# Performance work log

Measured on AMD Instinct MI355X. Metric: run time of the kernel, lower is better.

The kernel has to match this reference:

```python
import jax, jax.numpy as jnp
import numpy as np
from jax import lax

B, C_IN, N, C_OUT, K = 8, 64, 4096, 64, 20
EPS = 1e-5
NEG_SLOPE = 0.2


def setup_inputs() -> dict:
    key = jax.random.key(0)
    k1, k2, k3, k4, k5, k6 = jax.random.split(key, 6)
    x = jax.random.normal(k1, (B, C_IN, N), dtype=jnp.float32)
    # Conv2d(2*C_in, C_out, kernel_size=1, bias=False) -> weight (C_out, 2*C_in)
    W = jax.random.normal(k2, (C_OUT, 2 * C_IN), dtype=jnp.float32) * (1.0 / np.sqrt(2 * C_IN))
    gamma = jax.random.normal(k3, (C_OUT,), dtype=jnp.float32) * 0.1 + 1.0
    beta = jax.random.normal(k4, (C_OUT,), dtype=jnp.float32) * 0.1
    running_mean = jax.random.normal(k5, (C_OUT,), dtype=jnp.float32) * 0.1
    running_var = jax.random.uniform(k6, (C_OUT,), dtype=jnp.float32, minval=0.5, maxval=1.5)
    return {"x": x, "W": W, "gamma": gamma, "beta": beta,
            "running_mean": running_mean, "running_var": running_var}


def reference(x, W, gamma, beta, running_mean, running_var):
    # x: (B, C, N)
    # ---- KNN graph: pairwise squared distances, top-k nearest (includes self) ----
    xx = jnp.sum(x * x, axis=1)                       # (B, N)
    inner = jnp.einsum('bcn,bcm->bnm', x, x)          # (B, N, N)
    d2 = xx[:, :, None] - 2.0 * inner + xx[:, None, :]  # (B, N, N)
    _, idx = lax.top_k(-d2, K)                        # (B, N, K) int32 indices

    # ---- gather neighbor features ----
    xt = jnp.transpose(x, (0, 2, 1))                  # (B, N, C)
    neighbors = jax.vmap(lambda feats, i: feats[i])(xt, idx)  # (B, N, K, C)
    central = xt[:, :, None, :]                       # (B, N, 1, C) broadcast over K

    # ---- edge features: [x_i, x_j - x_i] -> (B, N, K, 2C) ----
    edge = jnp.concatenate(
        [jnp.broadcast_to(central, (B, N, K, C_IN)), neighbors - central], axis=-1)

    # ---- 1x1 conv (pointwise matmul) + BatchNorm (eval mode) + LeakyReLU ----
    h = jnp.einsum('bnkc,oc->bnko', edge, W)          # (B, N, K, C_out)
    inv_std = lax.rsqrt(running_var + EPS)
    h = (h - running_mean) * (inv_std * gamma) + beta
    h = jnp.where(h >= 0, h, NEG_SLOPE * h)           # LeakyReLU(0.2)

    # ---- max over k neighbors, return (B, C_out, N) ----
    out = jnp.max(h, axis=2)                          # (B, N, C_out)
    return jnp.transpose(out, (0, 2, 1))
```

## Files before the change

### kernel.cpp

```cpp
#include <hip/hip_runtime.h>

#define NB 8
#define NC 64
#define NN 4096
#define NO 64
#define KK 20
#define EPSV 1e-5f
#define SLOPE 0.2f

typedef __attribute__((ext_vector_type(8))) short short8x;
typedef __attribute__((ext_vector_type(4))) float float4x;


__device__ __forceinline__ unsigned short bfh(float f) {
  unsigned u = __float_as_uint(f);
  unsigned r = u + 0x7FFFu + ((u >> 16) & 1u);
  return (unsigned short)(r >> 16);
}

__device__ __forceinline__ unsigned flipf(float f) {
  unsigned u = __float_as_uint(f);
  return u ^ ((unsigned)((int)u >> 31) | 0x80000000u);
}

__global__ void k0_wprep(const float* __restrict__ W,
                         float* __restrict__ wa, float* __restrict__ wb) {
  int t = threadIdx.x;
  for (int i = t; i < NC * NO; i += 256) {
    int o = i & 63, c = i >> 6;
    float w1 = W[o * 128 + c];
    float w2 = W[o * 128 + 64 + c];
    wa[i] = w1 - w2;
    wb[i] = w2;
  }
}

__global__ __launch_bounds__(256) void k1_feat(const float* __restrict__ x,
    const float* __restrict__ waT, const float* __restrict__ wbT,
    float* __restrict__ y1, float* __restrict__ y2, float* __restrict__ xxg,
    unsigned short* __restrict__ xThi, unsigned short* __restrict__ xTmid,
    unsigned short* __restrict__ xTlo) {
  __shared__ __align__(16) float xs[NC * 68];
  __shared__ __align__(16) float wa[NC * NO];
  __shared__ __align__(16) float wb[NC * NO];
  int t = threadIdx.x;
  int b = blockIdx.x >> 6;
  int gr0 = (blockIdx.x & 63) << 6;
  const float* xb = x + (size_t)b * NC * NN;
  #pragma unroll
  for (int k = 0; k < 4; ++k) {
    int i4 = t + k * 256;
    int c = i4 >> 4, col4 = (i4 & 15) << 2;
    *(float4*)&xs[c * 68 + col4] = *(const float4*)&xb[(size_t)c * NN + gr0 + col4];
    *(float4*)&wa[c * 64 + col4] = *(const float4*)&waT[c * 64 + col4];
    *(float4*)&wb[c * 64 + col4] = *(const float4*)&wbT[c * 64 + col4];
  }
  __syncthreads();
  if (t < 64) {
    float s = 0.f;
    #pragma unroll
    for (int c = 0; c < NC; ++c) { float v = xs[c * 68 + t]; s = fmaf(v, v, s); }
    xxg[b * NN + gr0 + t] = s;
  }
  int o = t & 63, w = t >> 6;
  for (int j = 0; j < 16; ++j) {
    int n = j * 4 + w;
    float a1 = 0.f, a2 = 0.f;
    #pragma unroll
    for (int c = 0; c < NC; ++c) {
      float xv = xs[c * 68 + n];
      a1 = fmaf(wa[c * 64 + o], xv, a1);
      a2 = fmaf(wb[c * 64 + o], xv, a2);
    }
    size_t base = ((size_t)b * NN + gr0 + n) * NO + o;
    y1[base] = a1;
    y2[base] = a2;
  }
  int n2 = t >> 2, c0 = (t & 3) << 4;
  short8x vh[2], vm[2], vl[2];
  #pragma unroll
  for (int i = 0; i < 16; ++i) {
    float v = xs[(c0 + i) * 68 + n2];
    unsigned short h = bfh(v);
    float hf = __uint_as_float((unsigned)h << 16);
    float r1 = v - hf;
    unsigned short md = bfh(r1);
    float mf = __uint_as_float((unsigned)md << 16);
    unsigned short lo = bfh(r1 - mf);
    vh[i >> 3][i & 7] = (short)h;
    vm[i >> 3][i & 7] = (short)md;
    vl[i >> 3][i & 7] = (short)lo;
  }
  size_t tb = ((size_t)(b * NN + gr0 + n2)) * 64 + c0;
  *(short8x*)&xThi[tb] = vh[0];  *(short8x*)&xThi[tb + 8] = vh[1];
  *(short8x*)&xTmid[tb] = vm[0]; *(short8x*)&xTmid[tb + 8] = vm[1];
  *(short8x*)&xTlo[tb] = vl[0];  *(short8x*)&xTlo[tb + 8] = vl[1];
}

__global__ __launch_bounds__(256, 3) void k2_topk(
    const unsigned short* __restrict__ xThi, const unsigned short* __restrict__ xTmid,
    const unsigned short* __restrict__ xTlo, const float* __restrict__ xxg,
    unsigned* __restrict__ keyuG, unsigned short* __restrict__ idxG) {
  __shared__ __align__(16) unsigned short Rb[3 * 4096];
  __shared__ __align__(16) unsigned candU[4096];
  __shared__ __align__(16) float xxs[64];
  __shared__ unsigned cutq[256];

  int t = threadIdx.x;
  int blk = blockIdx.x;
  int b = blk >> 7;
  int rem = blk & 127;
  int rg = rem >> 1, half = rem & 1;
  int gr0 = rg << 6;
  int gc0 = half << 11;
  int w = t >> 6;
  int lm = t & 15;
  int quad = (t >> 4) & 3;
  int orow = t & 63, oq = t >> 6;

  size_t abase = ((size_t)(b * NN + gr0 + 16 * w + lm)) * 64;
  short8x Ah[2], Am[2], Al[2];
  #pragma unroll
  for (int ks = 0; ks < 2; ++ks) {
    int co = ks * 32 + quad * 8;
    Ah[ks] = *(const short8x*)&xThi[abase + co];
    Am[ks] = *(const short8x*)&xTmid[abase + co];
    Al[ks] = *(const short8x*)&xTlo[abase + co];
  }
  cutq[t] = 0xFFFFFFFFu;

  unsigned long long lst[KK];
  #pragma unroll
  for (int j = 0; j < KK; ++j) lst[j] = ~0ull;

  int rotr = orow & 31;
  size_t bbase = (size_t)(b * NN) * 64;

  for (int mt = 0; mt < 32; ++mt) {
    int gm0 = gc0 + (mt << 6);
    __syncthreads();
    #pragma unroll
    for (int lvl = 0; lvl < 3; ++lvl) {
      const unsigned short* src = (lvl == 0) ? xThi : (lvl == 1) ? xTmid : xTlo;
      unsigned short* dst = Rb + lvl * 4096;
      #pragma unroll
      for (int p = 0; p < 2; ++p) {
        int idx = p * 256 + t;
        int n = idx >> 3, o = idx & 7;
        *(short8x*)&dst[n * 64 + ((o + n) & 7) * 8] =
            *(const short8x*)&src[bbase + (size_t)(gm0 + n) * 64 + o * 8];
      }
    }
    if (t < 16) *(float4*)&xxs[t * 4] = *(const float4*)&xxg[b * NN + gm0 + t * 4];
    __syncthreads();

    float4x acc[4];
    #pragma unroll
    for (int j = 0; j < 4; ++j) acc[j] = (float4x){0.f, 0.f, 0.f, 0.f};

    const unsigned short* RbH = Rb;
    const unsigned short* RbM = Rb + 4096;
    const unsigned short* RbL = Rb + 8192;
    #pragma unroll
    for (int ks = 0; ks < 2; ++ks) {
      #pragma unroll
      for (int j = 0; j < 4; ++j) {
        int n = 16 * j + lm;
        int off = n * 64 + ((ks * 4 + quad + n) & 7) * 8;
        short8x bh = *(const short8x*)&RbH[off];
        short8x bm = *(const short8x*)&RbM[off];
        short8x bl = *(const short8x*)&RbL[off];
        acc[j] = __builtin_amdgcn_mfma_f32_16x16x32_bf16(Am[ks], bm, acc[j], 0, 0, 0);
        acc[j] = __builtin_amdgcn_mfma_f32_16x16x32_bf16(Ah[ks], bl, acc[j], 0, 0, 0);
        acc[j] = __builtin_amdgcn_mfma_f32_16x16x32_bf16(Al[ks], bh, acc[j], 0, 0, 0);
        acc[j] = __builtin_amdgcn_mfma_f32_16x16x32_bf16(Ah[ks], bm, acc[j], 0, 0, 0);
        acc[j] = __builtin_amdgcn_mfma_f32_16x16x32_bf16(Am[ks], bh, acc[j], 0, 0, 0);
        acc[j] = __builtin_amdgcn_mfma_f32_16x16x32_bf16(Ah[ks], bh, acc[j], 0, 0, 0);
      }
    }

    float xq[4];
    #pragma unroll
    for (int j = 0; j < 4; ++j) xq[j] = xxs[16 * j + lm];

    #pragma unroll
    for (int j = 0; j < 4; ++j) {
      int c = 16 * j + lm;
      #pragma unroll
      for (int q = 0; q < 4; ++q) {
        int rl = quad * 4 + q;
        int r = 16 * w + rl;
        float key = fmaf(-2.f, acc[j][q], xq[j]);
        int pos = (c & 32) | ((c + (r & 31)) & 31);
        candU[r * 64 + pos] = flipf(key);
      }
    }
    __syncthreads();

    unsigned rc0 = cutq[orow * 4 + 0], rc1 = cutq[orow * 4 + 1];
    unsigned rc2 = cutq[orow * 4 + 2], rc3 = cutq[orow * 4 + 3];
    unsigned thr = min(min(rc0, rc1), min(rc2, rc3));
    unsigned own19 = (unsigned)(lst[KK - 1] >> 12);
    thr = min(thr, own19);
    unsigned mask = 0;
    #pragma unroll
    for (int g = 0; g < 16; ++g) {
      int c = oq * 16 + g;
      int pos = (c & 32) | ((c + rotr) & 31);
      unsigned ku = candU[orow * 64 + pos];
      mask |= (unsigned)(ku <= thr) << g;
    }
    while (mask) {
      int e = __builtin_ctz(mask);
      mask &= mask - 1;
      int c = oq * 16 + e;
      int pos = (c & 32) | ((c + rotr) & 31);
      unsigned ku = candU[orow * 64 + pos];
      unsigned long long p = ((unsigned long long)ku << 12) | (unsigned)(gm0 + c);
      if (p < lst[KK - 1]) {
        #pragma unroll
        for (int j = KK - 1; j >= 1; --j) {
          bool sh = p < lst[j - 1];
          unsigned long long cur = (p < lst[j]) ? p : lst[j];
          lst[j] = sh ? lst[j - 1] : cur;
        }
        if (p < lst[0]) lst[0] = p;
      }
    }
    cutq[orow * 4 + oq] = (unsigned)(lst[KK - 1] >> 12);
  }

  unsigned long long* M = (unsigned long long*)Rb;
  #pragma unroll 1
  for (int ph = 0; ph < 2; ++ph) {
    __syncthreads();
    if ((orow >> 5) == ph) {
      int r5 = orow & 31;
      #pragma unroll
      for (int k = 0; k < KK; ++k) M[r5 * 84 + oq * 21 + k] = lst[k];
      M[r5 * 84 + oq * 21 + KK] = ~0ull;
    }
    __syncthreads();
    if (t < 32) {
      int h0 = 0, h1 = 0, h2 = 0, h3 = 0;
      int rb = t * 84;
      int row = ph * 32 + t;
      size_t base = ((size_t)(b * NN + gr0 + row) * 2 + half) * KK;
      for (int k = 0; k < KK; ++k) {
        unsigned long long v0 = M[rb + h0];
        unsigned long long v1 = M[rb + 21 + h1];
        unsigned long long v2 = M[rb + 42 + h2];
        unsigned long long v3 = M[rb + 63 + h3];
        unsigned long long bv = v0; int bq = 0;
        if (v1 < bv) { bv = v1; bq = 1; }
        if (v2 < bv) { bv = v2; bq = 2; }
        if (v3 < bv) { bv = v3; bq = 3; }
        keyuG[base + k] = (unsigned)(bv >> 12);
        idxG[base + k] = (unsigned short)(bv & 0xFFFu);
        if (bq == 0) h0++; else if (bq == 1) h1++; else if (bq == 2) h2++; else h3++;
      }
    }
  }
}

__global__ __launch_bounds__(256) void k3_out(const float* __restrict__ y1,
    const float* __restrict__ y2, const unsigned* __restrict__ keyuG,
    const unsigned short* __restrict__ idxG,
    const float* __restrict__ gamma, const float* __restrict__ beta,
    const float* __restrict__ rmean, const float* __restrict__ rvar,
    float* __restrict__ out) {
  __shared__ int sidx[64 * KK];
  __shared__ float ot[64 * 65];
  int t = threadIdx.x;
  int b = blockIdx.x >> 6;
  int gr0 = (blockIdx.x & 63) << 6;
  if (t < 64) {
    size_t base0 = ((size_t)(b * NN + gr0 + t) * 2) * KK;
    size_t base1 = base0 + KK;
    int h0 = 0, h1 = 0;
    for (int k = 0; k < KK; ++k) {
      int a0 = h0 < KK ? h0 : KK - 1;
      int a1 = h1 < KK ? h1 : KK - 1;
      unsigned k0v = keyuG[base0 + a0]; unsigned i0 = idxG[base0 + a0];
      unsigned k1v = keyuG[base1 + a1]; unsigned i1 = idxG[base1 + a1];
      bool take0 = (h1 >= KK) ||
                   ((h0 < KK) && (k0v < k1v || (k0v == k1v && i0 < i1)));
      sidx[t * KK + k] = take0 ? (int)i0 : (int)i1;
      if (take0) h0++; else h1++;
    }
  }
  int l = t & 63, w = t >> 6;
  float sc = gamma[l] * rsqrtf(rvar[l] + EPSV);
  float tt = fmaf(-rmean[l], sc, beta[l]);
  __syncthreads();
  const float* y2b = y2 + (size_t)b * NN * NO;
  for (int rr = 0; rr < 16; ++rr) {
    int row = w * 16 + rr;
    float v1 = y1[((size_t)b * NN + gr0 + row) * NO + l];
    int mk[KK];
    #pragma unroll
    for (int k = 0; k < KK; ++k) mk[k] = sidx[row * KK + k];
    float vv[KK];
    #pragma unroll
    for (int k = 0; k < KK; ++k) vv[k] = y2b[(size_t)mk[k] * NO + l];
    float best = -3.4e38f;
    #pragma unroll
    for (int k = 0; k < KK; ++k) {
      float v = v1 + vv[k];
      v = fmaf(v, sc, tt);
      v = v >= 0.f ? v : SLOPE * v;
      best = fmaxf(best, v);
    }
    ot[l * 65 + row] = best;
  }
  __syncthreads();
  float* ob = out + (size_t)b * NO * NN;
  for (int i = t; i < 4096; i += 256) {
    int o = i >> 6, n = i & 63;
    ob[(size_t)o * NN + gr0 + n] = ot[o * 65 + n];
  }
}

extern "C" void kernel_launch(void* const* d_in, const int* in_sizes, int n_in,
                              void* d_out, int out_size, void* d_ws, size_t ws_size,
                              hipStream_t stream) {
  const float* x     = (const float*)d_in[0];
  const float* W     = (const float*)d_in[1];
  const float* gamma = (const float*)d_in[2];
  const float* beta  = (const float*)d_in[3];
  const float* rmean = (const float*)d_in[4];
  const float* rvar  = (const float*)d_in[5];
  float* ws  = (float*)d_ws;
  float* y1    = ws;
  float* y2    = ws + 2097152;
  float* xx    = ws + 4194304;
  unsigned* keyu = (unsigned*)(ws + 4227072);
  unsigned short* idxu = (unsigned short*)(ws + 5537792);
  float* wa    = ws + 6193152;
  float* wb    = ws + 6197248;
  unsigned short* xThi  = (unsigned short*)(ws + 6201344);
  unsigned short* xTmid = (unsigned short*)(ws + 7249920);
  unsigned short* xTlo  = (unsigned short*)(ws + 8298496);
  float* out = (float*)d_out;

  hipLaunchKernelGGL(k0_wprep, dim3(1),    dim3(256), 0, stream, W, wa, wb);
  hipLaunchKernelGGL(k1_feat,  dim3(512),  dim3(256), 0, stream, x, wa, wb, y1, y2, xx,
                     xThi, xTmid, xTlo);
  hipLaunchKernelGGL(k2_topk,  dim3(1024), dim3(256), 0, stream, xThi, xTmid, xTlo,
                     xx, keyu, idxu);
  hipLaunchKernelGGL(k3_out,   dim3(512),  dim3(256), 0, stream, y1, y2, keyu, idxu,
                     gamma, beta, rmean, rvar, out);
}
```

Before: 406.4 us.

## Prefilter top-k candidates at MFMA output using per-row float cutoff bitmask

```diff
diff --git a/kernel.cpp b/kernel.cpp
--- a/kernel.cpp
+++ b/kernel.cpp
@@ -21,6 +21,10 @@
 __device__ __forceinline__ unsigned flipf(float f) {
   unsigned u = __float_as_uint(f);
   return u ^ ((unsigned)((int)u >> 31) | 0x80000000u);
+}
+
+__device__ __forceinline__ unsigned unflipu(unsigned v) {
+  return v ^ (0x80000000u | (unsigned)((int)(~v) >> 31));
 }
 
 __global__ void k0_wprep(const float* __restrict__ W,
@@ -105,6 +109,8 @@
   __shared__ __align__(16) unsigned candU[4096];
   __shared__ __align__(16) float xxs[64];
   __shared__ unsigned cutq[256];
+  __shared__ unsigned maskb[2 * 128];
+  __shared__ float cutminF[64];
 
   int t = threadIdx.x;
   int blk = blockIdx.x;
@@ -128,6 +134,8 @@
     Al[ks] = *(const short8x*)&xTlo[abase + co];
   }
   cutq[t] = 0xFFFFFFFFu;
+  maskb[t] = 0u;
+  if (t < 64) cutminF[t] = 3.4e38f;
 
   unsigned long long lst[KK];
   #pragma unroll
@@ -138,6 +146,7 @@
 
   for (int mt = 0; mt < 32; ++mt) {
     int gm0 = gc0 + (mt << 6);
+    int cur = mt & 1;
     __syncthreads();
     #pragma unroll
     for (int lvl = 0; lvl < 3; ++lvl) {
@@ -183,36 +192,38 @@
     #pragma unroll
     for (int j = 0; j < 4; ++j) xq[j] = xxs[16 * j + lm];
 
+    float cmf[4];
+    #pragma unroll
+    for (int q = 0; q < 4; ++q) cmf[q] = cutminF[16 * w + quad * 4 + q];
+    unsigned* mk = &maskb[cur * 128];
     #pragma unroll
     for (int j = 0; j < 4; ++j) {
       int c = 16 * j + lm;
       #pragma unroll
       for (int q = 0; q < 4; ++q) {
-        int rl = quad * 4 + q;
-        int r = 16 * w + rl;
+        int r = 16 * w + quad * 4 + q;
         float key = fmaf(-2.f, acc[j][q], xq[j]);
-        int pos = (c & 32) | ((c + (r & 31)) & 31);
-        candU[r * 64 + pos] = flipf(key);
-      }
-    }
-    __syncthreads();
-
-    unsigned rc0 = cutq[orow * 4 + 0], rc1 = cutq[orow * 4 + 1];
-    unsigned rc2 = cutq[orow * 4 + 2], rc3 = cutq[orow * 4 + 3];
-    unsigned thr = min(min(rc0, rc1), min(rc2, rc3));
-    unsigned own19 = (unsigned)(lst[KK - 1] >> 12);
-    thr = min(thr, own19);
-    unsigned mask = 0;
-    #pragma unroll
-    for (int g = 0; g < 16; ++g) {
-      int c = oq * 16 + g;
-      int pos = (c & 32) | ((c + rotr) & 31);
-      unsigned ku = candU[orow * 64 + pos];
-      mask |= (unsigned)(ku <= thr) << g;
-    }
-    while (mask) {
-      int e = __builtin_ctz(mask);
-      mask &= mask - 1;
+        if (key <= cmf[q]) {
+          int pos = (c & 32) | ((c + (r & 31)) & 31);
+          candU[r * 64 + pos] = flipf(key);
+          if (mt >= 2) atomicOr(&mk[r * 2 + (c >> 5)], 1u << (c & 31));
+        }
+      }
+    }
+    __syncthreads();
+
+    unsigned mbits;
+    if (mt < 2) {
+      mbits = 0xFFFFu;
+    } else {
+      unsigned word = maskb[cur * 128 + orow * 2 + (oq >> 1)];
+      mbits = (word >> ((oq & 1) * 16)) & 0xFFFFu;
+    }
+    if (t < 128) maskb[(cur ^ 1) * 128 + t] = 0u;
+
+    while (mbits) {
+      int e = __builtin_ctz(mbits);
+      mbits &= mbits - 1;
       int c = oq * 16 + e;
       int pos = (c & 32) | ((c + rotr) & 31);
       unsigned ku = candU[orow * 64 + pos];
@@ -221,13 +232,19 @@
         #pragma unroll
         for (int j = KK - 1; j >= 1; --j) {
           bool sh = p < lst[j - 1];
-          unsigned long long cur = (p < lst[j]) ? p : lst[j];
-          lst[j] = sh ? lst[j - 1] : cur;
+          unsigned long long curv = (p < lst[j]) ? p : lst[j];
+          lst[j] = sh ? lst[j - 1] : curv;
         }
         if (p < lst[0]) lst[0] = p;
       }
     }
     cutq[orow * 4 + oq] = (unsigned)(lst[KK - 1] >> 12);
+    if (t < 64) {
+      unsigned m0 = min(min(cutq[t * 4 + 0], cutq[t * 4 + 1]),
+                        min(cutq[t * 4 + 2], cutq[t * 4 + 3]));
+      m0 = min(m0, 0xFF7FFFFFu);
+      cutminF[t] = __uint_as_float(unflipu(m0));
+    }
   }
 
   unsigned long long* M = (unsigned long long*)Rb;
```

After: 479.8 us. 1.18x slower.
